# Kernel tuning notes

Hardware: AMD Instinct MI355X
Metric: run time of the kernel (lower is better)

Reference implementation:

```python
import jax, jax.numpy as jnp
import numpy as np

GAMMA = 0.002  # init kwarg
N, M, D = 8192, 8192, 512


def setup_inputs() -> dict:
    key = jax.random.key(0)
    kx, ky = jax.random.split(key)
    x = jax.random.normal(kx, (N, D), dtype=jnp.float32)
    y = jax.random.normal(ky, (M, D), dtype=jnp.float32)
    return {"x": x, "y": y}


def reference(x, y):
    # k(x, y) = exp(-gamma * ||x - y||^2), using the GEMM identity
    x = x.reshape(-1, x.shape[-1])
    y = y.reshape(-1, y.shape[-1])
    x_sq = jnp.sum(x * x, axis=-1)          # [N]
    y_sq = jnp.sum(y * y, axis=-1)          # [M]
    xy = jnp.einsum('nd,md->nm', x, y)      # [N, M] GEMM
    sq_dist = x_sq[:, None] + y_sq[None, :] - 2.0 * xy
    sq_dist = jnp.maximum(sq_dist, 0.0)     # clamp fp cancellation
    return jnp.exp(-jnp.float32(GAMMA) * sq_dist)
```

## Files before the change

### kernel.cpp

```cpp
#include <hip/hip_runtime.h>
#include <hip/hip_bf16.h>

#define GAMMA 0.002f
#define NROWS 8192
#define MROWS 8192
#define DDIM  512

typedef __attribute__((ext_vector_type(8))) short bf16x8;
typedef __attribute__((ext_vector_type(4))) float f32x4;
typedef __attribute__((ext_vector_type(8))) unsigned short ushort8;

static __device__ __forceinline__ unsigned short f32_to_bf16_rne(float f) {
    unsigned int u = __float_as_uint(f);
    unsigned int lsb = (u >> 16) & 1u;
    u += 0x7fffu + lsb;
    return (unsigned short)(u >> 16);
}

__global__ __launch_bounds__(64) void prep_kernel(const float* __restrict__ src,
                                                  unsigned short* __restrict__ dstb,
                                                  float* __restrict__ sq) {
    const int row  = blockIdx.x;
    const int lane = threadIdx.x;

    const float4* p = (const float4*)(src + (size_t)row * DDIM) + lane * 2;
    float4 f0 = p[0];
    float4 f1 = p[1];

    float s = f0.x*f0.x + f0.y*f0.y + f0.z*f0.z + f0.w*f0.w
            + f1.x*f1.x + f1.y*f1.y + f1.z*f1.z + f1.w*f1.w;

    float t[8] = {f0.x, f0.y, f0.z, f0.w, f1.x, f1.y, f1.z, f1.w};
    ushort8 hv;
#pragma unroll
    for (int i = 0; i < 8; ++i) hv[i] = f32_to_bf16_rne(t[i]);
    *(ushort8*)(dstb + (size_t)row * DDIM + lane * 8) = hv;

#pragma unroll
    for (int off = 32; off > 0; off >>= 1) s += __shfl_down(s, off);
    if (lane == 0) sq[row] = s;
}

__global__ __launch_bounds__(256) void rbf_gemm_kernel(
        const unsigned short* __restrict__ xb,
        const unsigned short* __restrict__ yb,
        const float* __restrict__ xsq,
        const float* __restrict__ ysq,
        float* __restrict__ out) {
    __shared__ __align__(16) unsigned short smem[2 * 128 * 32];
    unsigned short* smemA = smem;
    unsigned short* smemB = smem + 128 * 32;

    const int tid  = threadIdx.x;
    const int wave = tid >> 6;
    const int lane = tid & 63;

    const int rowBase = blockIdx.x * 128;
    const int colBase = blockIdx.y * 128;

    const int wm = wave >> 1;
    const int wn = wave & 1;

    f32x4 acc[4][4];
#pragma unroll
    for (int i = 0; i < 4; ++i)
#pragma unroll
        for (int j = 0; j < 4; ++j) acc[i][j] = (f32x4){0.f, 0.f, 0.f, 0.f};

    const int srow = lane >> 2;
    const int skb  = (lane & 3) * 16;

    const int fr  = lane & 15;
    const int fkb = (lane >> 4) * 16;

    for (int kt = 0; kt < DDIM / 32; ++kt) {
        const int k0b = kt * 64;
#pragma unroll
        for (int r = 0; r < 2; ++r) {
            const int seg = r * 4 + wave;
            {
                const char* g = (const char*)xb
                    + ((size_t)(rowBase + seg * 16 + srow) * DDIM) * 2 + k0b + skb;
                __builtin_amdgcn_global_load_lds(
                    (__attribute__((address_space(1))) void*)g,
                    (__attribute__((address_space(3))) void*)((char*)smemA + seg * 1024),
                    16, 0, 0);
            }
            {
                const char* g = (const char*)yb
                    + ((size_t)(colBase + seg * 16 + srow) * DDIM) * 2 + k0b + skb;
                __builtin_amdgcn_global_load_lds(
                    (__attribute__((address_space(1))) void*)g,
                    (__attribute__((address_space(3))) void*)((char*)smemB + seg * 1024),
                    16, 0, 0);
            }
        }
        __syncthreads();

        bf16x8 a[4], b[4];
#pragma unroll
        for (int i = 0; i < 4; ++i)
            a[i] = *(const bf16x8*)((const char*)smemA + (wm * 64 + i * 16 + fr) * 64 + fkb);
#pragma unroll
        for (int j = 0; j < 4; ++j)
            b[j] = *(const bf16x8*)((const char*)smemB + (wn * 64 + j * 16 + fr) * 64 + fkb);

#pragma unroll
        for (int i = 0; i < 4; ++i)
#pragma unroll
            for (int j = 0; j < 4; ++j)
                acc[i][j] = __builtin_amdgcn_mfma_f32_16x16x32_bf16(a[i], b[j], acc[i][j], 0, 0, 0);

        __syncthreads();
    }

    const int q4 = (lane >> 4) * 4;
#pragma unroll
    for (int i = 0; i < 4; ++i) {
        float xr[4];
#pragma unroll
        for (int r2 = 0; r2 < 4; ++r2)
            xr[r2] = xsq[rowBase + wm * 64 + i * 16 + q4 + r2];
#pragma unroll
        for (int j = 0; j < 4; ++j) {
            const int gcol = colBase + wn * 64 + j * 16 + fr;
            const float yc = ysq[gcol];
#pragma unroll
            for (int r2 = 0; r2 < 4; ++r2) {
                const int grow = rowBase + wm * 64 + i * 16 + q4 + r2;
                float d = xr[r2] + yc - 2.0f * acc[i][j][r2];
                d = fmaxf(d, 0.0f);
                out[(size_t)grow * MROWS + gcol] = __expf(-GAMMA * d);
            }
        }
    }
}

extern "C" void kernel_launch(void* const* d_in, const int* in_sizes, int n_in,
                              void* d_out, int out_size, void* d_ws, size_t ws_size,
                              hipStream_t stream) {
    const float* x = (const float*)d_in[0];
    const float* y = (const float*)d_in[1];
    float* out = (float*)d_out;

    unsigned short* xb = (unsigned short*)d_ws;
    unsigned short* yb = xb + (size_t)NROWS * DDIM;
    float* xsq = (float*)(yb + (size_t)MROWS * DDIM);
    float* ysq = xsq + NROWS;

    prep_kernel<<<NROWS, 64, 0, stream>>>(x, xb, xsq);
    prep_kernel<<<MROWS, 64, 0, stream>>>(y, yb, ysq);

    dim3 grid(NROWS / 128, MROWS / 128);
    rbf_gemm_kernel<<<grid, 256, 0, stream>>>(xb, yb, xsq, ysq, out);
}
```

Before: 353.9 us.

## Double K-tile to 64 with XOR-swizzled LDS and LDS-staged vectorized epilogue

Raises the K step per LDS tile from 32 to 64, which halves the number of barrier-separated iterations. It applies an XOR swizzle to the 16-byte chunk index so that the MFMA fragment reads from LDS avoid bank conflicts. The epilogue now writes exp results into per-wave LDS buffers (padded stride 68), then stores full rows as coalesced float4 writes instead of scattered scalar stores. Costs are double the LDS footprint and extra barriers in the epilogue.

```diff
diff --git a/kernel.cpp b/kernel.cpp
--- a/kernel.cpp
+++ b/kernel.cpp
@@ -47,9 +47,9 @@
         const float* __restrict__ xsq,
         const float* __restrict__ ysq,
         float* __restrict__ out) {
-    __shared__ __align__(16) unsigned short smem[2 * 128 * 32];
+    __shared__ __align__(16) unsigned short smem[2 * 128 * 64];
     unsigned short* smemA = smem;
-    unsigned short* smemB = smem + 128 * 32;
+    unsigned short* smemB = smem + 128 * 64;
 
     const int tid  = threadIdx.x;
     const int wave = tid >> 6;
@@ -67,20 +67,20 @@
 #pragma unroll
         for (int j = 0; j < 4; ++j) acc[i][j] = (f32x4){0.f, 0.f, 0.f, 0.f};
 
-    const int srow = lane >> 2;
-    const int skb  = (lane & 3) * 16;
+    const int srow   = lane >> 3;
+    const int schunk = (lane & 7) ^ srow;
 
-    const int fr  = lane & 15;
-    const int fkb = (lane >> 4) * 16;
+    const int fr = lane & 15;
+    const int q  = lane >> 4;
 
-    for (int kt = 0; kt < DDIM / 32; ++kt) {
-        const int k0b = kt * 64;
+    for (int kt = 0; kt < DDIM / 64; ++kt) {
 #pragma unroll
-        for (int r = 0; r < 2; ++r) {
+        for (int r = 0; r < 4; ++r) {
             const int seg = r * 4 + wave;
             {
                 const char* g = (const char*)xb
-                    + ((size_t)(rowBase + seg * 16 + srow) * DDIM) * 2 + k0b + skb;
+                    + (size_t)(rowBase + seg * 8 + srow) * (DDIM * 2)
+                    + kt * 128 + schunk * 16;
                 __builtin_amdgcn_global_load_lds(
                     (__attribute__((address_space(1))) void*)g,
                     (__attribute__((address_space(3))) void*)((char*)smemA + seg * 1024),
@@ -88,7 +88,8 @@
             }
             {
                 const char* g = (const char*)yb
-                    + ((size_t)(colBase + seg * 16 + srow) * DDIM) * 2 + k0b + skb;
+                    + (size_t)(colBase + seg * 8 + srow) * (DDIM * 2)
+                    + kt * 128 + schunk * 16;
                 __builtin_amdgcn_global_load_lds(
                     (__attribute__((address_space(1))) void*)g,
                     (__attribute__((address_space(3))) void*)((char*)smemB + seg * 1024),
@@ -97,41 +98,63 @@
         }
         __syncthreads();
 
-        bf16x8 a[4], b[4];
 #pragma unroll
-        for (int i = 0; i < 4; ++i)
-            a[i] = *(const bf16x8*)((const char*)smemA + (wm * 64 + i * 16 + fr) * 64 + fkb);
+        for (int k2 = 0; k2 < 2; ++k2) {
+            bf16x8 a[4], b[4];
 #pragma unroll
-        for (int j = 0; j < 4; ++j)
-            b[j] = *(const bf16x8*)((const char*)smemB + (wn * 64 + j * 16 + fr) * 64 + fkb);
-
+            for (int i = 0; i < 4; ++i) {
+                const int row = wm * 64 + i * 16 + fr;
+                const int ch  = (k2 * 4 + q) ^ (fr & 7);
+                a[i] = *(const bf16x8*)((const char*)smemA + row * 128 + ch * 16);
+            }
 #pragma unroll
-        for (int i = 0; i < 4; ++i)
+            for (int j = 0; j < 4; ++j) {
+                const int row = wn * 64 + j * 16 + fr;
+                const int ch  = (k2 * 4 + q) ^ (fr & 7);
+                b[j] = *(const bf16x8*)((const char*)smemB + row * 128 + ch * 16);
+            }
 #pragma unroll
-            for (int j = 0; j < 4; ++j)
-                acc[i][j] = __builtin_amdgcn_mfma_f32_16x16x32_bf16(a[i], b[j], acc[i][j], 0, 0, 0);
-
+            for (int i = 0; i < 4; ++i)
+#pragma unroll
+                for (int j = 0; j < 4; ++j)
+                    acc[i][j] = __builtin_amdgcn_mfma_f32_16x16x32_bf16(a[i], b[j], acc[i][j], 0, 0, 0);
+        }
         __syncthreads();
     }
 
-    const int q4 = (lane >> 4) * 4;
+    float* wbuf = (float*)smem + wave * (16 * 68);
+
+    float yc[4];
+#pragma unroll
+    for (int j = 0; j < 4; ++j) yc[j] = ysq[colBase + wn * 64 + j * 16 + fr];
+    const int q4 = q * 4;
+
 #pragma unroll
     for (int i = 0; i < 4; ++i) {
         float xr[4];
 #pragma unroll
         for (int r2 = 0; r2 < 4; ++r2)
             xr[r2] = xsq[rowBase + wm * 64 + i * 16 + q4 + r2];
+
+        __syncthreads();
 #pragma unroll
         for (int j = 0; j < 4; ++j) {
-            const int gcol = colBase + wn * 64 + j * 16 + fr;
-            const float yc = ysq[gcol];
 #pragma unroll
             for (int r2 = 0; r2 < 4; ++r2) {
-                const int grow = rowBase + wm * 64 + i * 16 + q4 + r2;
-                float d = xr[r2] + yc - 2.0f * acc[i][j][r2];
+                float d = xr[r2] + yc[j] - 2.0f * acc[i][j][r2];
                 d = fmaxf(d, 0.0f);
-                out[(size_t)grow * MROWS + gcol] = __expf(-GAMMA * d);
+                wbuf[(q4 + r2) * 68 + j * 16 + fr] = __expf(-GAMMA * d);
             }
+        }
+        __syncthreads();
+
+#pragma unroll
+        for (int p = 0; p < 4; ++p) {
+            const int lrow = p * 4 + q;
+            float4 v = *(const float4*)&wbuf[lrow * 68 + fr * 4];
+            const int grow = rowBase + wm * 64 + i * 16 + lrow;
+            const int gcol = colBase + wn * 64 + fr * 4;
+            *(float4*)(out + (size_t)grow * MROWS + gcol) = v;
         }
     }
 }
```

Measured after the change: 360.5 us. About the same (+1.9%).
